# Kernel tuning notes

Hardware: AMD Instinct MI355X
Metric: run time of the kernel (lower is better)

The kernel has to match this reference:

```python
import jax, jax.numpy as jnp
import numpy as np

THRESHOLD = 0.5
NEG_POS_RATIO = 3
VARIANCE = (0.1, 0.2)


def point_form(p):
    # center-form (cx,cy,w,h) -> corner-form (xmin,ymin,xmax,ymax)
    return jnp.concatenate([p[:, :2] - p[:, 2:] / 2, p[:, :2] + p[:, 2:] / 2], axis=-1)


def jaccard(a, b):
    # a: [N,4] corner boxes, b: [P,4] corner boxes -> IoU [N,P]
    lt = jnp.maximum(a[:, None, :2], b[None, :, :2])
    rb = jnp.minimum(a[:, None, 2:], b[None, :, 2:])
    wh = jnp.clip(rb - lt, 0.0)
    inter = wh[..., 0] * wh[..., 1]
    area_a = ((a[:, 2] - a[:, 0]) * (a[:, 3] - a[:, 1]))[:, None]
    area_b = ((b[:, 2] - b[:, 0]) * (b[:, 3] - b[:, 1]))[None, :]
    return inter / (area_a + area_b - inter)


def encode(matched, priors_cf):
    # matched: [P,4] corner GT boxes, priors_cf: [P,4] center-form priors
    g_cxcy = (matched[:, :2] + matched[:, 2:]) / 2 - priors_cf[:, :2]
    g_cxcy = g_cxcy / (VARIANCE[0] * priors_cf[:, 2:])
    g_wh = jnp.log((matched[:, 2:] - matched[:, :2]) / priors_cf[:, 2:]) / VARIANCE[1]
    return jnp.concatenate([g_cxcy, g_wh], axis=-1)  # [P,4]


def match_one(truths, labels, priors_cf):
    # truths: [N,4], labels: [N], priors_cf: [P,4]
    n_obj = truths.shape[0]
    overlaps = jaccard(truths, point_form(priors_cf))          # [N,P]
    best_prior_idx = jnp.argmax(overlaps, axis=1)              # [N] best prior per GT
    best_truth_overlap = jnp.max(overlaps, axis=0)             # [P]
    best_truth_idx = jnp.argmax(overlaps, axis=0)              # [P] best GT per prior
    # ensure every GT keeps its best prior
    best_truth_overlap = best_truth_overlap.at[best_prior_idx].set(2.0)
    best_truth_idx = best_truth_idx.at[best_prior_idx].set(jnp.arange(n_obj))
    matched = truths[best_truth_idx]                           # [P,4]
    conf = jnp.where(best_truth_overlap < THRESHOLD, 0, labels[best_truth_idx] + 1)
    return encode(matched, priors_cf), conf.astype(jnp.int32)


def setup_inputs() -> dict:
    key = jax.random.key(0)
    k1, k2, k3, k4, k5, k6, k7 = jax.random.split(key, 7)
    B, P, C, NOBJ = 64, 24564, 21, 32
    loc_data = jax.random.normal(k1, (B, P, 4), jnp.float32)
    conf_data = jax.random.normal(k2, (B, P, C), jnp.float32)
    p_cxcy = jax.random.uniform(k3, (P, 2), jnp.float32, 0.05, 0.95)
    p_wh = jax.random.uniform(k4, (P, 2), jnp.float32, 0.02, 0.4)
    priors = jnp.concatenate([p_cxcy, p_wh], axis=-1)          # center-form
    t_cxcy = jax.random.uniform(k5, (B, NOBJ, 2), jnp.float32, 0.2, 0.8)
    t_wh = jax.random.uniform(k6, (B, NOBJ, 2), jnp.float32, 0.05, 0.3)
    targets_boxes = jnp.concatenate([t_cxcy - t_wh / 2, t_cxcy + t_wh / 2], axis=-1)
    targets_labels = jax.random.randint(k7, (B, NOBJ), 0, C - 1)  # 0..19, +1 in match
    return {
        "loc_data": loc_data,
        "conf_data": conf_data,
        "priors": priors,
        "targets_boxes": targets_boxes,
        "targets_labels": targets_labels,
    }


def reference(loc_data, conf_data, priors, targets_boxes, targets_labels):
    B, P, C = conf_data.shape
    # targets/priors are detached in the original (.data)
    loc_t, conf_t = jax.vmap(match_one, in_axes=(0, 0, None))(
        jax.lax.stop_gradient(targets_boxes), targets_labels,
        jax.lax.stop_gradient(priors))                          # [B,P,4], [B,P]

    pos = conf_t > 0                                            # [B,P]
    num_pos = jnp.sum(pos, axis=1)                              # [B]

    # localization: smooth L1 on positives, summed
    diff = loc_data - loc_t
    ad = jnp.abs(diff)
    sl1 = jnp.where(ad < 1.0, 0.5 * diff * diff, ad - 0.5)      # [B,P,4]
    loss_l = jnp.sum(sl1 * pos[..., None].astype(sl1.dtype))

    # confidence cross-entropy per prior: lse(x) - x[target]
    lse = jax.nn.logsumexp(conf_data, axis=-1)                  # [B,P]
    gathered = jnp.take_along_axis(conf_data, conf_t[..., None], axis=-1)[..., 0]
    ce_all = lse - gathered                                     # [B,P]

    # hard negative mining: rank negatives by loss, keep top 3*num_pos
    loss_mine = jnp.where(pos, 0.0, ce_all)
    order = jnp.argsort(-loss_mine, axis=1)
    idx_rank = jnp.argsort(order, axis=1)                       # rank of each prior
    num_neg = jnp.clip(NEG_POS_RATIO * num_pos, 0, P - 1)       # [B]
    neg = idx_rank < num_neg[:, None]

    mask = jnp.logical_or(pos, neg)
    loss_c = jnp.sum(ce_all * mask.astype(ce_all.dtype))

    N = jnp.maximum(jnp.sum(num_pos), 1).astype(loss_l.dtype)
    return jnp.stack([loss_l / N, loss_c / N])
```

## Files before the change

kernel.cpp:

```cpp
#include <hip/hip_runtime.h>
#include <stdint.h>

#define THRESH 0.5f
#define VAR0 0.1f
#define VAR1 0.2f

typedef float f4u __attribute__((ext_vector_type(4), aligned(4)));

__global__ __launch_bounds__(256, 8) void fused_kernel(
    const float* __restrict__ loc_data, const float* __restrict__ conf_data,
    const float* __restrict__ priors, const float* __restrict__ tboxes,
    const int* __restrict__ labels,
    unsigned long long* __restrict__ part_best,
    float* __restrict__ loss_mine,
    float* __restrict__ ll_part, float* __restrict__ pc_part,
    int* __restrict__ np_part, unsigned int* __restrict__ done_ctr,
    int P, int C, int NOBJ, int NBLK)
{
#pragma clang fp contract(off)
    __shared__ float siou[16 * 260];
    __shared__ float spv[32][17];
    __shared__ unsigned char sps[32][20];
    __shared__ float ta[32];
    __shared__ float sll[4], spc[4];
    __shared__ int snp[4];

    const int b = blockIdx.y, bx = blockIdx.x, tid = threadIdx.x;
    const int p0 = bx * 256;
    const int p = p0 + tid;
    const int rows = min(256, P - p0);
    if (b == 0 && bx == 0 && tid == 0) *done_ctr = 0;

    const float4* tb = (const float4*)tboxes + (size_t)b * NOBJ;

    const bool fastC = (C == 21);
    const float* row = conf_data + ((size_t)b * P + p) * C;
    const bool havefast = fastC && (tid < rows);
    f4u a0, a1, a2, a3, a4;
    float a5 = 0.f;
    if (havefast) {
        const f4u* r4 = (const f4u*)row;
        a0 = r4[0]; a1 = r4[1]; a2 = r4[2]; a3 = r4[3]; a4 = r4[4];
        a5 = row[20];
    }

    if (tid < NOBJ) {
        float4 t = tb[tid];
        ta[tid] = (t.z - t.x) * (t.w - t.y);
    }
    __syncthreads();

    float s_pre = 0.f;
    if (havefast) {
        float s;
        s  = __expf(a0.x); s += __expf(a0.y); s += __expf(a0.z); s += __expf(a0.w);
        s += __expf(a1.x); s += __expf(a1.y); s += __expf(a1.z); s += __expf(a1.w);
        s += __expf(a2.x); s += __expf(a2.y); s += __expf(a2.z); s += __expf(a2.w);
        s += __expf(a3.x); s += __expf(a3.y); s += __expf(a3.z); s += __expf(a3.w);
        s += __expf(a4.x); s += __expf(a4.y); s += __expf(a4.z); s += __expf(a4.w);
        s += __expf(a5);
        s_pre = s;
    } else if (tid < rows) {
        float s = 0.f;
        for (int j = 0; j < C; ++j) s += __expf(row[j]);
        s_pre = s;
    }
    asm volatile("" : "+v"(s_pre));

    const bool valid = (p < P);
    float ax = 0.f, ay = 0.f, bxx = 0.f, byy = 0.f, area_p = 0.f;
    if (valid) {
        float4 pr = ((const float4*)priors)[p];
        ax = pr.x - pr.z * 0.5f;
        ay = pr.y - pr.w * 0.5f;
        bxx = pr.x + pr.z * 0.5f;
        byy = pr.y + pr.w * 0.5f;
        area_p = (bxx - ax) * (byy - ay);
    }

    float bestv = -1.0f;
    int bestn = 0;
    for (int n0 = 0; n0 < NOBJ; n0 += 16) {
        const int jmax = min(16, NOBJ - n0);
#pragma unroll 4
        for (int j = 0; j < jmax; ++j) {
            float4 t = tb[n0 + j];
            float iou = -1.0f;
            if (valid) {
                float w = fminf(t.z, bxx) - fmaxf(t.x, ax); if (w < 0.f) w = 0.f;
                float h = fminf(t.w, byy) - fmaxf(t.y, ay); if (h < 0.f) h = 0.f;
                float inter = w * h;
                float denom = (ta[n0 + j] + area_p) - inter;
                iou = inter * __builtin_amdgcn_rcpf(denom);
                if (iou > bestv) { bestv = iou; bestn = n0 + j; }
            }
            siou[j * 260 + tid] = iou;
        }
        __syncthreads();
        {
            const int n2 = tid & 15, c = tid >> 4;
            if (n2 < jmax) {
                float bv = -1.0f;
                int bs = 0;
                const int base = n2 * 260 + c;
                for (int j2 = 0; j2 < 16; ++j2) {
                    float v = siou[base + (j2 << 4)];
                    if (v > bv) { bv = v; bs = (j2 << 4) + c; }
                }
                spv[n0 + n2][c] = bv;
                sps[n0 + n2][c] = (unsigned char)bs;
            }
        }
        __syncthreads();
    }
    if (tid < NOBJ) {
        float bv = -1.0f;
        int bs = 0;
        for (int c2 = 0; c2 < 16; ++c2) {
            float v = spv[tid][c2];
            int s2 = (int)sps[tid][c2];
            if (v > bv || (v == bv && s2 < bs)) { bv = v; bs = s2; }
        }
        unsigned long long pk = 0ULL;
        if (bv >= 0.f) {
            unsigned int pp = (unsigned int)(p0 + bs);
            pk = (((unsigned long long)__float_as_uint(bv)) << 32) |
                 (unsigned long long)(0xFFFFFFFFu - pp);
        }
        part_best[((size_t)b * NBLK + bx) * NOBJ + tid] = pk;
    }

    float ll = 0.f, pc = 0.f;
    int np = 0;
    if (tid < rows) {
        const size_t g = (size_t)b * P + p;
        int conf_t = (bestv < THRESH) ? 0 : labels[b * NOBJ + bestn] + 1;

        float ce = __logf(s_pre) - conf_data[g * (size_t)C + conf_t];

        bool pos = (conf_t > 0);
        loss_mine[g] = pos ? 0.f : ce;
        if (pos) {
            np = 1;
            pc = ce;
            float4 t = tb[bestn];
            float4 pr = ((const float4*)priors)[p];
            float gcx = ((t.x + t.z) * 0.5f - pr.x) / (VAR0 * pr.z);
            float gcy = ((t.y + t.w) * 0.5f - pr.y) / (VAR0 * pr.w);
            float gw  = __logf((t.z - t.x) / pr.z) / VAR1;
            float gh  = __logf((t.w - t.y) / pr.w) / VAR1;
            float4 ld = ((const float4*)loc_data)[g];
            float d, a;
            d = ld.x - gcx; a = fabsf(d); ll += (a < 1.f) ? 0.5f * d * d : a - 0.5f;
            d = ld.y - gcy; a = fabsf(d); ll += (a < 1.f) ? 0.5f * d * d : a - 0.5f;
            d = ld.z - gw;  a = fabsf(d); ll += (a < 1.f) ? 0.5f * d * d : a - 0.5f;
            d = ld.w - gh;  a = fabsf(d); ll += (a < 1.f) ? 0.5f * d * d : a - 0.5f;
        }
    }

    for (int off = 32; off; off >>= 1) {
        ll += __shfl_down(ll, off, 64);
        pc += __shfl_down(pc, off, 64);
        np += __shfl_down(np, off, 64);
    }
    const int lane = tid & 63, wid = tid >> 6;
    if (lane == 0) { sll[wid] = ll; spc[wid] = pc; snp[wid] = np; }
    __syncthreads();
    if (tid == 0) {
        size_t slot = (size_t)b * NBLK + bx;
        ll_part[slot] = sll[0] + sll[1] + sll[2] + sll[3];
        pc_part[slot] = spc[0] + spc[1] + spc[2] + spc[3];
        np_part[slot] = snp[0] + snp[1] + snp[2] + snp[3];
    }
}

__global__ __launch_bounds__(1024) void selectcf_kernel(
    const float* __restrict__ loc_data, const float* __restrict__ conf_data,
    const float* __restrict__ priors, const float* __restrict__ tboxes,
    const int* __restrict__ labels,
    const unsigned long long* __restrict__ part_best,
    float* __restrict__ loss_mine,
    const float* __restrict__ ll_part, const float* __restrict__ pc_part,
    const int* __restrict__ np_part,
    double* __restrict__ neg, double* __restrict__ dll_b,
    double* __restrict__ dpc_b, int* __restrict__ npos_b,
    unsigned int* __restrict__ done_ctr, float* __restrict__ out,
    int P, int C, int NOBJ, int NBLK, int B, int ratio)
{
#pragma clang fp contract(off)
    const int b = blockIdx.x;
    const int tid = threadIdx.x;
    const int lane = tid & 63, wid = tid >> 6;

    __shared__ float4 tr[32];
    __shared__ unsigned long long sp2[32][17];
    __shared__ unsigned long long bb[32];
    __shared__ int2 centry[32];
    __shared__ double sdll[32], sdpc[32];
    __shared__ int cnt_s, snp_s, snp_corr;
    __shared__ unsigned int hist[16][257];
    __shared__ unsigned int merged[256];
    __shared__ unsigned int sh_sel, sh_k;
    __shared__ double sd[16];
    __shared__ unsigned int sc[16];
    __shared__ double negv_s;
    __shared__ int is_last_s;

    if (tid == 0) { cnt_s = 0; snp_s = 0; snp_corr = 0; negv_s = 0.0; }
    if (tid < NOBJ) tr[tid] = ((const float4*)tboxes)[(size_t)b * NOBJ + tid];
    __syncthreads();

    if (tid < NBLK) atomicAdd(&snp_s, np_part[b * NBLK + tid]);

    {
        const int n = tid & 31, c = tid >> 5;
        if (tid < 512 && n < NOBJ) {
            unsigned long long best = 0ULL;
            for (int j = c; j < NBLK; j += 16) {
                unsigned long long v = part_best[((size_t)b * NBLK + j) * NOBJ + n];
                if (v > best) best = v;
            }
            sp2[n][c] = best;
        }
    }
    __syncthreads();
    if (tid < NOBJ) {
        unsigned long long best = 0ULL;
        for (int c = 0; c < 16; ++c) {
            unsigned long long v = sp2[tid][c];
            if (v > best) best = v;
        }
        bb[tid] = best;
    }
    __syncthreads();

    if (wid == 0) {
        const bool have = (lane < NOBJ);
        unsigned int mypidx = have
            ? (0xFFFFFFFFu - (unsigned int)(bb[lane] & 0xFFFFFFFFu))
            : (0x80000000u + (unsigned int)lane);
        bool dead = false;
        for (int m = 0; m < NOBJ; ++m) {
            unsigned int o = __shfl(mypidx, m, 64);
            if (m > lane && o == mypidx) dead = true;
        }
        unsigned long long win = __ballot(have && !dead);
        if (have && !dead) {
            int rank = (int)__popcll(win & ((1ULL << lane) - 1ULL));
            centry[rank] = make_int2((int)mypidx, lane);
        }
        if (lane == 0) cnt_s = (int)__popcll(win);
    }
    __syncthreads();

    if (tid < cnt_s) {
        const int pidx = centry[tid].x;
        const int n = centry[tid].y;
        float4 pr = ((const float4*)priors)[pidx];
        float ax = pr.x - pr.z * 0.5f;
        float ay = pr.y - pr.w * 0.5f;
        float bxx = pr.x + pr.z * 0.5f;
        float byy = pr.y + pr.w * 0.5f;
        float area_p = (bxx - ax) * (byy - ay);
        float bestv = -1.0f;
        int bestn = 0;
        for (int nn = 0; nn < NOBJ; ++nn) {
            float4 t = tr[nn];
            float w = fminf(t.z, bxx) - fmaxf(t.x, ax); if (w < 0.f) w = 0.f;
            float h = fminf(t.w, byy) - fmaxf(t.y, ay); if (h < 0.f) h = 0.f;
            float inter = w * h;
            float att = (t.z - t.x) * (t.w - t.y);
            float denom = (att + area_p) - inter;
            float iou = inter * __builtin_amdgcn_rcpf(denom);
            if (iou > bestv) { bestv = iou; bestn = nn; }
        }
        const float* row = conf_data + ((size_t)b * P + pidx) * C;
        float s = 0.f;
        for (int j = 0; j < C; ++j) s += __expf(row[j]);
        float lse = __logf(s);

        int old_conf = (bestv < THRESH) ? 0 : labels[b * NOBJ + bestn] + 1;
        int new_conf = labels[b * NOBJ + n] + 1;
        bool old_pos = (old_conf > 0);

        double dpc = old_pos ? ((double)row[old_conf] - (double)row[new_conf])
                             : (double)(lse - row[new_conf]);

        const size_t g = (size_t)b * P + pidx;
        float4 ld = ((const float4*)loc_data)[g];
        float sl1_new, sl1_old = 0.f;
        {
            float4 t = tr[n];
            float gcx = ((t.x + t.z) * 0.5f - pr.x) / (VAR0 * pr.z);
            float gcy = ((t.y + t.w) * 0.5f - pr.y) / (VAR0 * pr.w);
            float gw  = __logf((t.z - t.x) / pr.z) / VAR1;
            float gh  = __logf((t.w - t.y) / pr.w) / VAR1;
            float ll = 0.f, d, a;
            d = ld.x - gcx; a = fabsf(d); ll += (a < 1.f) ? 0.5f * d * d : a - 0.5f;
            d = ld.y - gcy; a = fabsf(d); ll += (a < 1.f) ? 0.5f * d * d : a - 0.5f;
            d = ld.z - gw;  a = fabsf(d); ll += (a < 1.f) ? 0.5f * d * d : a - 0.5f;
            d = ld.w - gh;  a = fabsf(d); ll += (a < 1.f) ? 0.5f * d * d : a - 0.5f;
            sl1_new = ll;
        }
        if (old_pos) {
            float4 t = tr[bestn];
            float gcx = ((t.x + t.z) * 0.5f - pr.x) / (VAR0 * pr.z);
            float gcy = ((t.y + t.w) * 0.5f - pr.y) / (VAR0 * pr.w);
            float gw  = __logf((t.z - t.x) / pr.z) / VAR1;
            float gh  = __logf((t.w - t.y) / pr.w) / VAR1;
            float ll = 0.f, d, a;
            d = ld.x - gcx; a = fabsf(d); ll += (a < 1.f) ? 0.5f * d * d : a - 0.5f;
            d = ld.y - gcy; a = fabsf(d); ll += (a < 1.f) ? 0.5f * d * d : a - 0.5f;
            d = ld.z - gw;  a = fabsf(d); ll += (a < 1.f) ? 0.5f * d * d : a - 0.5f;
            d = ld.w - gh;  a = fabsf(d); ll += (a < 1.f) ? 0.5f * d * d : a - 0.5f;
            sl1_old = ll;
        }
        sdll[tid] = (double)sl1_new - (double)sl1_old;
        sdpc[tid] = dpc;
        if (!old_pos) {
            atomicAdd(&snp_corr, 1);
            loss_mine[g] = 0.f;
        }
    }
    __syncthreads();

    int k = ratio * (snp_s + snp_corr);
    if (k > P - 1) k = P - 1;

    if (k > 0) {
        const f4u* fv4 = (const f4u*)(loss_mine + (size_t)b * P);
        const int P4 = P >> 2;
        const int tail0 = P4 << 2;
        unsigned int prefix = 0, mask = 0;
        unsigned int kk = (unsigned int)k;
        for (int shift = 24; shift >= 0; shift -= 8) {
            for (int t = tid; t < 16 * 257; t += 1024) (&hist[0][0])[t] = 0;
            __syncthreads();
            unsigned int* h = hist[wid];
            for (int i4 = tid; i4 < P4; i4 += 1024) {
                f4u v4 = fv4[i4];
                unsigned int v;
                v = __float_as_uint(v4.x);
                if ((v & mask) == prefix) atomicAdd(&h[(v >> shift) & 255u], 1u);
                v = __float_as_uint(v4.y);
                if ((v & mask) == prefix) atomicAdd(&h[(v >> shift) & 255u], 1u);
                v = __float_as_uint(v4.z);
                if ((v & mask) == prefix) atomicAdd(&h[(v >> shift) & 255u], 1u);
                v = __float_as_uint(v4.w);
                if ((v & mask) == prefix) atomicAdd(&h[(v >> shift) & 255u], 1u);
            }
            for (int i = tail0 + tid; i < P; i += 1024) {
                unsigned int v = __float_as_uint(loss_mine[(size_t)b * P + i]);
                if ((v & mask) == prefix) atomicAdd(&h[(v >> shift) & 255u], 1u);
            }
            __syncthreads();
            if (tid < 256) {
                unsigned int s = 0;
                for (int w = 0; w < 16; ++w) s += hist[w][tid];
                merged[tid] = s;
            }
            __syncthreads();
            if (wid == 0) {
                unsigned int h0 = merged[4 * lane], h1 = merged[4 * lane + 1];
                unsigned int h2 = merged[4 * lane + 2], h3 = merged[4 * lane + 3];
                unsigned int s3 = h3, s2 = h2 + s3, s1 = h1 + s2, s0 = h0 + s1;
                unsigned int t = s0;
                unsigned int T = t;
                for (int off = 1; off < 64; off <<= 1) {
                    unsigned int o = __shfl_down(T, off, 64);
                    if (lane + off < 64) T += o;
                }
                unsigned int A = T - t;
                unsigned int S0 = A + s0, S1 = A + s1, S2 = A + s2, S3 = A + s3, S4 = A;
                if (S0 >= kk && S1 < kk) { sh_sel = 4 * lane + 0; sh_k = kk - S1; }
                if (S1 >= kk && S2 < kk) { sh_sel = 4 * lane + 1; sh_k = kk - S2; }
                if (S2 >= kk && S3 < kk) { sh_sel = 4 * lane + 2; sh_k = kk - S3; }
                if (S3 >= kk && S4 < kk) { sh_sel = 4 * lane + 3; sh_k = kk - S4; }
            }
            __syncthreads();
            prefix |= sh_sel << shift;
            mask |= 0xFFu << shift;
            kk = sh_k;
        }
        const float T = __uint_as_float(prefix);

        double sum = 0.0;
        unsigned int cnt = 0;
        for (int i4 = tid; i4 < P4; i4 += 1024) {
            f4u v4 = fv4[i4];
            if (v4.x > T) { sum += (double)v4.x; cnt++; }
            if (v4.y > T) { sum += (double)v4.y; cnt++; }
            if (v4.z > T) { sum += (double)v4.z; cnt++; }
            if (v4.w > T) { sum += (double)v4.w; cnt++; }
        }
        for (int i = tail0 + tid; i < P; i += 1024) {
            float v = loss_mine[(size_t)b * P + i];
            if (v > T) { sum += (double)v; cnt++; }
        }
        for (int off = 32; off; off >>= 1) {
            sum += __shfl_down(sum, off, 64);
            cnt += __shfl_down(cnt, off, 64);
        }
        if (lane == 0) { sd[wid] = sum; sc[wid] = cnt; }
        __syncthreads();
        if (tid == 0) {
            double S = 0.0;
            unsigned int Cn = 0;
            for (int w = 0; w < 16; ++w) { S += sd[w]; Cn += sc[w]; }
            negv_s = S + (double)((unsigned int)k - Cn) * (double)T;
        }
    }
    __syncthreads();

    if (tid == 0) {
        double DL = 0.0, DP = 0.0;
        for (int j = 0; j < cnt_s; ++j) { DL += sdll[j]; DP += sdpc[j]; }
        neg[b] = negv_s;
        dll_b[b] = DL;
        dpc_b[b] = DP;
        npos_b[b] = snp_s + snp_corr;
        __threadfence();
        unsigned int old = atomicAdd(done_ctr, 1u);
        is_last_s = (old == (unsigned int)B - 1) ? 1 : 0;
    }
    __syncthreads();
    if (!is_last_s) return;
    __threadfence();

    double LL = 0.0, PC = 0.0, NG = 0.0;
    long long NP = 0;
    const int NPART = B * NBLK;
    for (int i = tid; i < NPART; i += 1024) {
        LL += (double)ll_part[i];
        PC += (double)pc_part[i];
    }
    for (int i = tid; i < B; i += 1024) {
        NG += neg[i];
        LL += dll_b[i];
        PC += dpc_b[i];
        NP += (long long)npos_b[i];
    }
    for (int off = 32; off; off >>= 1) {
        LL += __shfl_down(LL, off, 64);
        PC += __shfl_down(PC, off, 64);
        NG += __shfl_down(NG, off, 64);
        NP += __shfl_down(NP, off, 64);
    }
    __shared__ double fll[16], fpc[16], fng[16];
    __shared__ long long fnp[16];
    if (lane == 0) { fll[wid] = LL; fpc[wid] = PC; fng[wid] = NG; fnp[wid] = NP; }
    __syncthreads();
    if (tid == 0) {
        double L = 0.0, Pc = 0.0, Ng = 0.0;
        long long Np = 0;
        for (int w = 0; w < 16; ++w) { L += fll[w]; Pc += fpc[w]; Ng += fng[w]; Np += fnp[w]; }
        if (Np < 1) Np = 1;
        double N = (double)Np;
        out[0] = (float)(L / N);
        out[1] = (float)((Pc + Ng) / N);
    }
}

extern "C" void kernel_launch(void* const* d_in, const int* in_sizes, int n_in,
                              void* d_out, int out_size, void* d_ws, size_t ws_size,
                              hipStream_t stream)
{
    const float* loc_data  = (const float*)d_in[0];
    const float* conf_data = (const float*)d_in[1];
    const float* priors    = (const float*)d_in[2];
    const float* tboxes    = (const float*)d_in[3];
    const int*   tlabels   = (const int*)d_in[4];

    const int P = in_sizes[2] / 4;
    const int B = (int)((long long)in_sizes[0] / ((long long)P * 4));
    const int C = (int)((long long)in_sizes[1] / ((long long)B * P));
    const int NOBJ = in_sizes[4] / B;
    const int NBLK = (P + 255) / 256;

    char* ws = (char*)d_ws;
    size_t off = 0;
    unsigned int* done_ctr = (unsigned int*)(ws + off);  off += 256;
    double* neg = (double*)(ws + off);                   off += (size_t)B * 8;
    off = (off + 255) & ~(size_t)255;
    double* dll_b = (double*)(ws + off);                 off += (size_t)B * 8;
    off = (off + 255) & ~(size_t)255;
    double* dpc_b = (double*)(ws + off);                 off += (size_t)B * 8;
    off = (off + 255) & ~(size_t)255;
    int* npos_b = (int*)(ws + off);                      off += (size_t)B * 4;
    off = (off + 255) & ~(size_t)255;
    float* ll_part = (float*)(ws + off);                 off += (size_t)B * NBLK * 4;
    off = (off + 255) & ~(size_t)255;
    float* pc_part = (float*)(ws + off);                 off += (size_t)B * NBLK * 4;
    off = (off + 255) & ~(size_t)255;
    int* np_part = (int*)(ws + off);                     off += (size_t)B * NBLK * 4;
    off = (off + 255) & ~(size_t)255;
    unsigned long long* part_best = (unsigned long long*)(ws + off);
    off += (size_t)B * NBLK * NOBJ * 8;
    off = (off + 255) & ~(size_t)255;
    float* loss_mine = (float*)(ws + off);

    dim3 grid(NBLK, B);
    fused_kernel<<<grid, 256, 0, stream>>>(
        loc_data, conf_data, priors, tboxes, tlabels,
        part_best, loss_mine, ll_part, pc_part, np_part, done_ctr,
        P, C, NOBJ, NBLK);
    selectcf_kernel<<<B, 1024, 0, stream>>>(
        loc_data, conf_data, priors, tboxes, tlabels,
        part_best, loss_mine, ll_part, pc_part, np_part,
        neg, dll_b, dpc_b, npos_b, done_ctr, (float*)d_out,
        P, C, NOBJ, NBLK, B, 3);
}
```

Before: 276.1 us.

## Compact radix-select candidates into LDS after second pass

After the second 8-bit radix pass, each block collects the values matching the 16-bit prefix into a shared-memory buffer. It also accumulates the sum and count of values above that prefix. The last two histogram passes and the final threshold sum then read the compact LDS buffer instead of rescanning loss_mine in global memory. When candidates exceed the buffer capacity it falls back to the global scans, and the extra compaction pass adds atomics and LDS usage.

After: 275.6 us. Within noise of the previous version (-0.2%).

```diff
diff --git a/kernel.cpp b/kernel.cpp
--- a/kernel.cpp
+++ b/kernel.cpp
@@ -4,6 +4,7 @@
 #define THRESH 0.5f
 #define VAR0 0.1f
 #define VAR1 0.2f
+#define CAP 6144
 
 typedef float f4u __attribute__((ext_vector_type(4), aligned(4)));
 
@@ -201,6 +202,8 @@
     __shared__ unsigned int hist[16][257];
     __shared__ unsigned int merged[256];
     __shared__ unsigned int sh_sel, sh_k;
+    __shared__ float cbuf[CAP];
+    __shared__ int ccnt;
     __shared__ double sd[16];
     __shared__ unsigned int sc[16];
     __shared__ double negv_s;
@@ -333,25 +336,37 @@
         const int tail0 = P4 << 2;
         unsigned int prefix = 0, mask = 0;
         unsigned int kk = (unsigned int)k;
+        int ncand = -1;
+        double psum = 0.0;
+        unsigned int pcnt = 0;
+
         for (int shift = 24; shift >= 0; shift -= 8) {
             for (int t = tid; t < 16 * 257; t += 1024) (&hist[0][0])[t] = 0;
             __syncthreads();
             unsigned int* h = hist[wid];
-            for (int i4 = tid; i4 < P4; i4 += 1024) {
-                f4u v4 = fv4[i4];
-                unsigned int v;
-                v = __float_as_uint(v4.x);
-                if ((v & mask) == prefix) atomicAdd(&h[(v >> shift) & 255u], 1u);
-                v = __float_as_uint(v4.y);
-                if ((v & mask) == prefix) atomicAdd(&h[(v >> shift) & 255u], 1u);
-                v = __float_as_uint(v4.z);
-                if ((v & mask) == prefix) atomicAdd(&h[(v >> shift) & 255u], 1u);
-                v = __float_as_uint(v4.w);
-                if ((v & mask) == prefix) atomicAdd(&h[(v >> shift) & 255u], 1u);
-            }
-            for (int i = tail0 + tid; i < P; i += 1024) {
-                unsigned int v = __float_as_uint(loss_mine[(size_t)b * P + i]);
-                if ((v & mask) == prefix) atomicAdd(&h[(v >> shift) & 255u], 1u);
+            const bool lds_src = (ncand >= 0) && (ncand <= CAP);
+            if (lds_src) {
+                for (int i = tid; i < ncand; i += 1024) {
+                    unsigned int v = __float_as_uint(cbuf[i]);
+                    if ((v & mask) == prefix) atomicAdd(&h[(v >> shift) & 255u], 1u);
+                }
+            } else {
+                for (int i4 = tid; i4 < P4; i4 += 1024) {
+                    f4u v4 = fv4[i4];
+                    unsigned int v;
+                    v = __float_as_uint(v4.x);
+                    if ((v & mask) == prefix) atomicAdd(&h[(v >> shift) & 255u], 1u);
+                    v = __float_as_uint(v4.y);
+                    if ((v & mask) == prefix) atomicAdd(&h[(v >> shift) & 255u], 1u);
+                    v = __float_as_uint(v4.z);
+                    if ((v & mask) == prefix) atomicAdd(&h[(v >> shift) & 255u], 1u);
+                    v = __float_as_uint(v4.w);
+                    if ((v & mask) == prefix) atomicAdd(&h[(v >> shift) & 255u], 1u);
+                }
+                for (int i = tail0 + tid; i < P; i += 1024) {
+                    unsigned int v = __float_as_uint(loss_mine[(size_t)b * P + i]);
+                    if ((v & mask) == prefix) atomicAdd(&h[(v >> shift) & 255u], 1u);
+                }
             }
             __syncthreads();
             if (tid < 256) {
@@ -381,21 +396,60 @@
             prefix |= sh_sel << shift;
             mask |= 0xFFu << shift;
             kk = sh_k;
+
+            if (shift == 16) {
+                if (tid == 0) ccnt = 0;
+                __syncthreads();
+                for (int i4 = tid; i4 < P4; i4 += 1024) {
+                    f4u v4 = fv4[i4];
+                    unsigned int v, pf;
+                    v = __float_as_uint(v4.x); pf = v & 0xFFFF0000u;
+                    if (pf == prefix) { int s_ = atomicAdd(&ccnt, 1); if (s_ < CAP) cbuf[s_] = v4.x; }
+                    else if (pf > prefix) { psum += (double)v4.x; pcnt++; }
+                    v = __float_as_uint(v4.y); pf = v & 0xFFFF0000u;
+                    if (pf == prefix) { int s_ = atomicAdd(&ccnt, 1); if (s_ < CAP) cbuf[s_] = v4.y; }
+                    else if (pf > prefix) { psum += (double)v4.y; pcnt++; }
+                    v = __float_as_uint(v4.z); pf = v & 0xFFFF0000u;
+                    if (pf == prefix) { int s_ = atomicAdd(&ccnt, 1); if (s_ < CAP) cbuf[s_] = v4.z; }
+                    else if (pf > prefix) { psum += (double)v4.z; pcnt++; }
+                    v = __float_as_uint(v4.w); pf = v & 0xFFFF0000u;
+                    if (pf == prefix) { int s_ = atomicAdd(&ccnt, 1); if (s_ < CAP) cbuf[s_] = v4.w; }
+                    else if (pf > prefix) { psum += (double)v4.w; pcnt++; }
+                }
+                for (int i = tail0 + tid; i < P; i += 1024) {
+                    float fvv = loss_mine[(size_t)b * P + i];
+                    unsigned int v = __float_as_uint(fvv);
+                    unsigned int pf = v & 0xFFFF0000u;
+                    if (pf == prefix) { int s_ = atomicAdd(&ccnt, 1); if (s_ < CAP) cbuf[s_] = fvv; }
+                    else if (pf > prefix) { psum += (double)fvv; pcnt++; }
+                }
+                __syncthreads();
+                ncand = ccnt;
+            }
         }
         const float T = __uint_as_float(prefix);
 
-        double sum = 0.0;
-        unsigned int cnt = 0;
-        for (int i4 = tid; i4 < P4; i4 += 1024) {
-            f4u v4 = fv4[i4];
-            if (v4.x > T) { sum += (double)v4.x; cnt++; }
-            if (v4.y > T) { sum += (double)v4.y; cnt++; }
-            if (v4.z > T) { sum += (double)v4.z; cnt++; }
-            if (v4.w > T) { sum += (double)v4.w; cnt++; }
-        }
-        for (int i = tail0 + tid; i < P; i += 1024) {
-            float v = loss_mine[(size_t)b * P + i];
-            if (v > T) { sum += (double)v; cnt++; }
+        double sum;
+        unsigned int cnt;
+        if (ncand >= 0 && ncand <= CAP) {
+            sum = psum; cnt = pcnt;
+            for (int i = tid; i < ncand; i += 1024) {
+                float v = cbuf[i];
+                if (v > T) { sum += (double)v; cnt++; }
+            }
+        } else {
+            sum = 0.0; cnt = 0;
+            for (int i4 = tid; i4 < P4; i4 += 1024) {
+                f4u v4 = fv4[i4];
+                if (v4.x > T) { sum += (double)v4.x; cnt++; }
+                if (v4.y > T) { sum += (double)v4.y; cnt++; }
+                if (v4.z > T) { sum += (double)v4.z; cnt++; }
+                if (v4.w > T) { sum += (double)v4.w; cnt++; }
+            }
+            for (int i = tail0 + tid; i < P; i += 1024) {
+                float v = loss_mine[(size_t)b * P + i];
+                if (v > T) { sum += (double)v; cnt++; }
+            }
         }
         for (int off = 32; off; off >>= 1) {
             sum += __shfl_down(sum, off, 64);
```
